# Optimization experiments

Hardware: AMD Instinct MI355X
Metric: run time of the kernel (lower is better)

The kernel has to match this reference:

```python
import jax, jax.numpy as jnp
import numpy as np

ALPHA = 0.2        # LeakyReLU slope
NEG_BIG = -9e15    # mask fill value from the original module


def setup_inputs() -> dict:
    key = jax.random.key(0)
    k1, k2, k3, k4 = jax.random.split(key, 4)
    N, F_IN, F_OUT = 8192, 256, 128
    h = jax.random.normal(k1, (N, F_IN), dtype=jnp.float32)
    adj = jax.random.randint(k2, (N, N), 0, 2, dtype=jnp.int32)
    W = jax.random.normal(k3, (F_IN, F_OUT), dtype=jnp.float32) * (1.0 / np.sqrt(F_IN))
    a = jax.random.normal(k4, (2 * F_OUT, 1), dtype=jnp.float32) * (1.0 / np.sqrt(2 * F_OUT))
    return {"h": h, "adj": adj, "W": W, "a": a}


def reference(h, adj, W, a):
    f_out = W.shape[1]
    Wh = h @ W                                   # [N, F_out]
    Wh1 = Wh @ a[:f_out, :]                      # [N, 1]
    Wh2 = Wh @ a[f_out:, :]                      # [N, 1]
    e = Wh1 + Wh2.T                              # [N, N] broadcast-add
    e = jnp.where(e > 0, e, ALPHA * e)           # LeakyReLU
    e = jnp.where(adj > 0, e, NEG_BIG)           # adjacency mask
    attention = jax.nn.softmax(e, axis=-1)       # row softmax
    # dropout rate = 0.0 -> identity
    h_prime = attention @ Wh                     # [N, F_out]
    return jax.nn.elu(h_prime)
```

## Files before the change

### kernel.cpp

```cpp
#include <hip/hip_runtime.h>

#define NV 8192
#define FIN 256
#define FOUT 128
#define NSPLIT 8
#define SPLITW 1024

typedef __bf16 bf16_t;
typedef __attribute__((ext_vector_type(8))) __bf16 bf16x8;
typedef __attribute__((ext_vector_type(16))) float f32x16;

__global__ __launch_bounds__(256) void wh_kernel(
    const float* __restrict__ h, const float* __restrict__ W,
    const float* __restrict__ a,
    bf16_t* __restrict__ WhbT,
    float* __restrict__ E1, float* __restrict__ F1,
    float* __restrict__ E2, float* __restrict__ F2)
{
  __shared__ float As[64][34];
  __shared__ float Bs[64][128];
  __shared__ float Cs[32][129];
  __shared__ float red1[32][16];
  __shared__ float red2[32][16];
  const int t  = threadIdx.x;
  const int i0 = blockIdx.x * 32;
  const int c  = t & 15;
  const int r  = t >> 4;
  float acc0[8], acc1[8];
  #pragma unroll
  for (int j = 0; j < 8; j++) { acc0[j] = 0.f; acc1[j] = 0.f; }

  for (int k0 = 0; k0 < FIN; k0 += 64) {
    {
      const int ia = t >> 3;
      const int ka = (t & 7) * 8;
      const float* src = h + (size_t)(i0 + ia) * FIN + k0 + ka;
      float4 v0 = *(const float4*)src;
      float4 v1 = *(const float4*)(src + 4);
      As[ka+0][ia]=v0.x; As[ka+1][ia]=v0.y; As[ka+2][ia]=v0.z; As[ka+3][ia]=v0.w;
      As[ka+4][ia]=v1.x; As[ka+5][ia]=v1.y; As[ka+6][ia]=v1.z; As[ka+7][ia]=v1.w;
    }
    {
      const int kb = t >> 2;
      const int cb = (t & 3) * 32;
      const float4* src = (const float4*)(W + (size_t)(k0 + kb) * FOUT + cb);
      float4* dst = (float4*)&Bs[kb][cb];
      #pragma unroll
      for (int q = 0; q < 8; q++) dst[q] = src[q];
    }
    __syncthreads();
    #pragma unroll 4
    for (int k = 0; k < 64; k++) {
      float2 av = *(const float2*)&As[k][r*2];
      float b[8];
      *(float4*)&b[0] = *(const float4*)&Bs[k][c*8];
      *(float4*)&b[4] = *(const float4*)&Bs[k][c*8+4];
      #pragma unroll
      for (int j = 0; j < 8; j++) {
        acc0[j] = fmaf(av.x, b[j], acc0[j]);
        acc1[j] = fmaf(av.y, b[j], acc1[j]);
      }
    }
    __syncthreads();
  }

  float p1a = 0.f, p2a = 0.f, p1b = 0.f, p2b = 0.f;
  #pragma unroll
  for (int j = 0; j < 8; j++) {
    Cs[r*2][c*8+j]   = acc0[j];
    Cs[r*2+1][c*8+j] = acc1[j];
    float w1 = a[c*8+j];
    float w2 = a[FOUT + c*8+j];
    p1a = fmaf(acc0[j], w1, p1a); p2a = fmaf(acc0[j], w2, p2a);
    p1b = fmaf(acc1[j], w1, p1b); p2b = fmaf(acc1[j], w2, p2b);
  }
  red1[r*2][c]   = p1a; red2[r*2][c]   = p2a;
  red1[r*2+1][c] = p1b; red2[r*2+1][c] = p2b;
  __syncthreads();
  if (t < 32) {
    float s = 0.f;
    #pragma unroll
    for (int q = 0; q < 16; q++) s += red1[t][q];
    E1[i0 + t] = __expf(s);
    F1[i0 + t] = __expf(0.2f * s);
  } else if (t < 64) {
    float s = 0.f;
    #pragma unroll
    for (int q = 0; q < 16; q++) s += red2[t-32][q];
    E2[i0 + t - 32] = __expf(s);
    F2[i0 + t - 32] = __expf(0.2f * s);
  }
  {
    const int f = t & 127, half = t >> 7;
    union { bf16_t b[16]; uint4 v[2]; } pk;
    #pragma unroll
    for (int q = 0; q < 16; q++) pk.b[q] = (bf16_t)Cs[half*16 + q][f];
    uint4* dst = (uint4*)(WhbT + (size_t)f * NV + i0 + half*16);
    dst[0] = pk.v[0]; dst[1] = pk.v[1];
  }
}

__global__ __launch_bounds__(256, 3) void attn_kernel(
    const int* __restrict__ adj, const bf16_t* __restrict__ WhbT,
    const float* __restrict__ E1v, const float* __restrict__ F1v,
    const float* __restrict__ E2v, const float* __restrict__ F2v,
    float* __restrict__ nump, float* __restrict__ denp)
{
  __shared__ bf16_t Plds[64][72];
  __shared__ bf16_t Blds[2][128][72];
  __shared__ float denlds[64][4];
  const int t     = threadIdx.x;
  const int rb    = blockIdx.x >> 3;
  const int split = blockIdx.x & 7;
  const int i0 = rb * 64;
  const int j0 = split * SPLITW;
  const int il = t >> 2;
  const int jg = (t & 3) * 16;
  const float e1 = E1v[i0 + il];
  const float f1 = F1v[i0 + il];
  const int lane = t & 63;
  const int w    = t >> 6;
  const int rh = (w & 1) * 32;
  const int ch = (w >> 1) * 64;
  const int ml = lane & 31;
  const int kh = (lane >> 5) * 8;
  f32x16 acc0 = {};
  f32x16 acc1 = {};
  float den_t = 0.f;

  const int bn  = t >> 1;
  const int bhf = (t & 1) * 32;
  const bf16_t* bsrc = WhbT + (size_t)bn * NV + j0 + bhf;
  const int* arow = adj + (size_t)(i0 + il) * NV + j0 + jg;

  uint4 br0, br1, br2, br3;
  {
    const uint4* s4 = (const uint4*)bsrc;
    br0 = s4[0]; br1 = s4[1]; br2 = s4[2]; br3 = s4[3];
  }
  int4 ca0 = *(const int4*)(arow + 0);
  int4 ca1 = *(const int4*)(arow + 4);
  int4 ca2 = *(const int4*)(arow + 8);
  int4 ca3 = *(const int4*)(arow + 12);

  for (int jc = 0; jc < SPLITW; jc += 64) {
    const int jb  = j0 + jc;
    const int buf = (jc >> 6) & 1;
    {
      uint4* bd = (uint4*)&Blds[buf][bn][bhf];
      bd[0] = br0; bd[1] = br1; bd[2] = br2; bd[3] = br3;
    }
    float4 w0 = *(const float4*)(E2v + jb + jg);
    float4 w1 = *(const float4*)(E2v + jb + jg + 4);
    float4 w2 = *(const float4*)(E2v + jb + jg + 8);
    float4 w3 = *(const float4*)(E2v + jb + jg + 12);
    float4 x0 = *(const float4*)(F2v + jb + jg);
    float4 x1 = *(const float4*)(F2v + jb + jg + 4);
    float4 x2 = *(const float4*)(F2v + jb + jg + 8);
    float4 x3 = *(const float4*)(F2v + jb + jg + 12);
    const int jn = (jc + 64 < SPLITW) ? jc + 64 : jc;
    {
      const uint4* s4 = (const uint4*)(bsrc + jn);
      br0 = s4[0]; br1 = s4[1]; br2 = s4[2]; br3 = s4[3];
    }
    const int* nrow = arow + jn;
    int4 na0 = *(const int4*)(nrow + 0);
    int4 na1 = *(const int4*)(nrow + 4);
    int4 na2 = *(const int4*)(nrow + 8);
    int4 na3 = *(const int4*)(nrow + 12);
    {
      bf16x8 pv0, pv1;
      float d0 = 0.f, d1 = 0.f, d2 = 0.f, d3 = 0.f;
      #define PGRP(CA, E4, F4, DD, PV, SL) { \
        float px = fmaxf(e1*E4.x, f1*F4.x); px = (CA.x > 0) ? px : 0.f; DD += px; PV[SL+0] = (bf16_t)px; \
        float py = fmaxf(e1*E4.y, f1*F4.y); py = (CA.y > 0) ? py : 0.f; DD += py; PV[SL+1] = (bf16_t)py; \
        float pz = fmaxf(e1*E4.z, f1*F4.z); pz = (CA.z > 0) ? pz : 0.f; DD += pz; PV[SL+2] = (bf16_t)pz; \
        float pw = fmaxf(e1*E4.w, f1*F4.w); pw = (CA.w > 0) ? pw : 0.f; DD += pw; PV[SL+3] = (bf16_t)pw; }
      PGRP(ca0, w0, x0, d0, pv0, 0)
      PGRP(ca1, w1, x1, d1, pv0, 4)
      PGRP(ca2, w2, x2, d2, pv1, 0)
      PGRP(ca3, w3, x3, d3, pv1, 4)
      #undef PGRP
      den_t += (d0 + d1) + (d2 + d3);
      *(bf16x8*)&Plds[il][jg]     = pv0;
      *(bf16x8*)&Plds[il][jg + 8] = pv1;
    }
    asm volatile("s_waitcnt lgkmcnt(0)\n\ts_barrier" ::: "memory");
    #pragma unroll
    for (int ks = 0; ks < 4; ks++) {
      const int k = ks * 16 + kh;
      bf16x8 af = *(const bf16x8*)&Plds[rh + ml][k];
      bf16x8 b0 = *(const bf16x8*)&Blds[buf][ch + ml][k];
      bf16x8 b1 = *(const bf16x8*)&Blds[buf][ch + 32 + ml][k];
      acc0 = __builtin_amdgcn_mfma_f32_32x32x16_bf16(af, b0, acc0, 0, 0, 0);
      acc1 = __builtin_amdgcn_mfma_f32_32x32x16_bf16(af, b1, acc1, 0, 0, 0);
    }
    asm volatile("s_barrier" ::: "memory");
    ca0 = na0; ca1 = na1; ca2 = na2; ca3 = na3;
  }

  denlds[il][t & 3] = den_t;
  __syncthreads();
  if (t < 64) {
    denp[(size_t)split * NV + i0 + t] =
        denlds[t][0] + denlds[t][1] + denlds[t][2] + denlds[t][3];
  }
  float* base = nump + ((size_t)split * NV + i0) * FOUT;
  const int col = ch + ml;
  const int r4  = 4 * (lane >> 5);
  #pragma unroll
  for (int reg = 0; reg < 16; reg++) {
    const int row = rh + (reg & 3) + 8 * (reg >> 2) + r4;
    base[(size_t)row * FOUT + col]      = acc0[reg];
    base[(size_t)row * FOUT + col + 32] = acc1[reg];
  }
}

__global__ __launch_bounds__(256) void finalize_kernel(
    const float* __restrict__ nump, const float* __restrict__ denp,
    float* __restrict__ out)
{
  const int gid = blockIdx.x * 256 + threadIdx.x;
  const int i  = gid >> 5;
  const int f0 = (gid & 31) * 4;
  float den = 0.f;
  #pragma unroll
  for (int sp = 0; sp < NSPLIT; sp++) den += denp[(size_t)sp * NV + i];
  float4 s = make_float4(0.f, 0.f, 0.f, 0.f);
  #pragma unroll
  for (int sp = 0; sp < NSPLIT; sp++) {
    float4 v = *(const float4*)&nump[((size_t)sp * NV + i) * FOUT + f0];
    s.x += v.x; s.y += v.y; s.z += v.z; s.w += v.w;
  }
  const float inv = 1.0f / den;
  float4 r;
  r.x = s.x * inv; r.y = s.y * inv; r.z = s.z * inv; r.w = s.w * inv;
  r.x = r.x > 0.f ? r.x : __expf(r.x) - 1.0f;
  r.y = r.y > 0.f ? r.y : __expf(r.y) - 1.0f;
  r.z = r.z > 0.f ? r.z : __expf(r.z) - 1.0f;
  r.w = r.w > 0.f ? r.w : __expf(r.w) - 1.0f;
  *(float4*)&out[(size_t)i * FOUT + f0] = r;
}

extern "C" void kernel_launch(void* const* d_in, const int* in_sizes, int n_in,
                              void* d_out, int out_size, void* d_ws, size_t ws_size,
                              hipStream_t stream) {
  const float* h  = (const float*)d_in[0];
  const int*  adj = (const int*)d_in[1];
  const float* W  = (const float*)d_in[2];
  const float* a  = (const float*)d_in[3];
  float* out = (float*)d_out;
  char* ws = (char*)d_ws;
  bf16_t* WhbT = (bf16_t*)ws;
  float* E1   = (float*)(ws + 2097152);
  float* F1   = (float*)(ws + 2129920);
  float* E2   = (float*)(ws + 2162688);
  float* F2   = (float*)(ws + 2195456);
  float* denp = (float*)(ws + 2228224);
  float* nump = (float*)(ws + 2490368);

  wh_kernel<<<256, 256, 0, stream>>>(h, W, a, WhbT, E1, F1, E2, F2);
  attn_kernel<<<1024, 256, 0, stream>>>(adj, WhbT, E1, F1, E2, F2, nump, denp);
  finalize_kernel<<<1024, 256, 0, stream>>>(nump, denp, out);
}
```

Baseline: 417.6 us.

## Pack adjacency mask into bitmask in a separate pass before attention

Adds a pack kernel that converts the int32 adjacency matrix into one bit per edge. The attention kernel then reads one 32-bit word per thread per tile instead of sixteen int32 values, and tests bits for masking. This takes the large adjacency stream out of the MFMA-heavy kernel and lightens its loads and register use. The cost is an extra kernel launch that still reads the full adjacency matrix and writes the bit array to the workspace.

```diff
diff --git a/kernel.cpp b/kernel.cpp
--- a/kernel.cpp
+++ b/kernel.cpp
@@ -5,10 +5,34 @@
 #define FOUT 128
 #define NSPLIT 8
 #define SPLITW 1024
+#define NW32 256
 
 typedef __bf16 bf16_t;
 typedef __attribute__((ext_vector_type(8))) __bf16 bf16x8;
 typedef __attribute__((ext_vector_type(16))) float f32x16;
+
+__global__ __launch_bounds__(256) void pack_kernel(
+    const int* __restrict__ adj, unsigned* __restrict__ bits)
+{
+  const int g0 = (blockIdx.x * 256 + threadIdx.x) * 4;
+  unsigned ob[4];
+  #pragma unroll
+  for (int k = 0; k < 4; k++) {
+    const int* src = adj + (size_t)(g0 + k) * 32;
+    unsigned b = 0;
+    #pragma unroll
+    for (int q = 0; q < 8; q++) {
+      int4 v = *(const int4*)(src + q * 4);
+      b |= (v.x > 0) ? (1u << (q * 4 + 0)) : 0u;
+      b |= (v.y > 0) ? (1u << (q * 4 + 1)) : 0u;
+      b |= (v.z > 0) ? (1u << (q * 4 + 2)) : 0u;
+      b |= (v.w > 0) ? (1u << (q * 4 + 3)) : 0u;
+    }
+    ob[k] = b;
+  }
+  uint4 o = make_uint4(ob[0], ob[1], ob[2], ob[3]);
+  *(uint4*)(bits + g0) = o;
+}
 
 __global__ __launch_bounds__(256) void wh_kernel(
     const float* __restrict__ h, const float* __restrict__ W,
@@ -101,7 +125,7 @@
 }
 
 __global__ __launch_bounds__(256, 3) void attn_kernel(
-    const int* __restrict__ adj, const bf16_t* __restrict__ WhbT,
+    const unsigned* __restrict__ abits, const bf16_t* __restrict__ WhbT,
     const float* __restrict__ E1v, const float* __restrict__ F1v,
     const float* __restrict__ E2v, const float* __restrict__ F2v,
     float* __restrict__ nump, float* __restrict__ denp)
@@ -124,6 +148,7 @@
   const int ch = (w >> 1) * 64;
   const int ml = lane & 31;
   const int kh = (lane >> 5) * 8;
+  const int bb = jg & 16;
   f32x16 acc0 = {};
   f32x16 acc1 = {};
   float den_t = 0.f;
@@ -131,17 +156,14 @@
   const int bn  = t >> 1;
   const int bhf = (t & 1) * 32;
   const bf16_t* bsrc = WhbT + (size_t)bn * NV + j0 + bhf;
-  const int* arow = adj + (size_t)(i0 + il) * NV + j0 + jg;
+  const unsigned* arow32 = abits + (size_t)(i0 + il) * NW32 + ((j0 + jg) >> 5);
 
   uint4 br0, br1, br2, br3;
   {
     const uint4* s4 = (const uint4*)bsrc;
     br0 = s4[0]; br1 = s4[1]; br2 = s4[2]; br3 = s4[3];
   }
-  int4 ca0 = *(const int4*)(arow + 0);
-  int4 ca1 = *(const int4*)(arow + 4);
-  int4 ca2 = *(const int4*)(arow + 8);
-  int4 ca3 = *(const int4*)(arow + 12);
+  unsigned cbits = arow32[0];
 
   for (int jc = 0; jc < SPLITW; jc += 64) {
     const int jb  = j0 + jc;
@@ -163,23 +185,20 @@
       const uint4* s4 = (const uint4*)(bsrc + jn);
       br0 = s4[0]; br1 = s4[1]; br2 = s4[2]; br3 = s4[3];
     }
-    const int* nrow = arow + jn;
-    int4 na0 = *(const int4*)(nrow + 0);
-    int4 na1 = *(const int4*)(nrow + 4);
-    int4 na2 = *(const int4*)(nrow + 8);
-    int4 na3 = *(const int4*)(nrow + 12);
-    {
+    unsigned nbits = arow32[jn >> 5];
+    {
+      const unsigned hb = cbits >> bb;
       bf16x8 pv0, pv1;
       float d0 = 0.f, d1 = 0.f, d2 = 0.f, d3 = 0.f;
-      #define PGRP(CA, E4, F4, DD, PV, SL) { \
-        float px = fmaxf(e1*E4.x, f1*F4.x); px = (CA.x > 0) ? px : 0.f; DD += px; PV[SL+0] = (bf16_t)px; \
-        float py = fmaxf(e1*E4.y, f1*F4.y); py = (CA.y > 0) ? py : 0.f; DD += py; PV[SL+1] = (bf16_t)py; \
-        float pz = fmaxf(e1*E4.z, f1*F4.z); pz = (CA.z > 0) ? pz : 0.f; DD += pz; PV[SL+2] = (bf16_t)pz; \
-        float pw = fmaxf(e1*E4.w, f1*F4.w); pw = (CA.w > 0) ? pw : 0.f; DD += pw; PV[SL+3] = (bf16_t)pw; }
-      PGRP(ca0, w0, x0, d0, pv0, 0)
-      PGRP(ca1, w1, x1, d1, pv0, 4)
-      PGRP(ca2, w2, x2, d2, pv1, 0)
-      PGRP(ca3, w3, x3, d3, pv1, 4)
+      #define PGRP(B, E4, F4, DD, PV, SL) { \
+        float px = fmaxf(e1*E4.x, f1*F4.x); px = (hb & (1u<<(B+0))) ? px : 0.f; DD += px; PV[SL+0] = (bf16_t)px; \
+        float py = fmaxf(e1*E4.y, f1*F4.y); py = (hb & (1u<<(B+1))) ? py : 0.f; DD += py; PV[SL+1] = (bf16_t)py; \
+        float pz = fmaxf(e1*E4.z, f1*F4.z); pz = (hb & (1u<<(B+2))) ? pz : 0.f; DD += pz; PV[SL+2] = (bf16_t)pz; \
+        float pw = fmaxf(e1*E4.w, f1*F4.w); pw = (hb & (1u<<(B+3))) ? pw : 0.f; DD += pw; PV[SL+3] = (bf16_t)pw; }
+      PGRP( 0, w0, x0, d0, pv0, 0)
+      PGRP( 4, w1, x1, d1, pv0, 4)
+      PGRP( 8, w2, x2, d2, pv1, 0)
+      PGRP(12, w3, x3, d3, pv1, 4)
       #undef PGRP
       den_t += (d0 + d1) + (d2 + d3);
       *(bf16x8*)&Plds[il][jg]     = pv0;
@@ -196,7 +215,7 @@
       acc1 = __builtin_amdgcn_mfma_f32_32x32x16_bf16(af, b1, acc1, 0, 0, 0);
     }
     asm volatile("s_barrier" ::: "memory");
-    ca0 = na0; ca1 = na1; ca2 = na2; ca3 = na3;
+    cbits = nbits;
   }
 
   denlds[il][t & 3] = den_t;
@@ -258,8 +277,10 @@
   float* F2   = (float*)(ws + 2195456);
   float* denp = (float*)(ws + 2228224);
   float* nump = (float*)(ws + 2490368);
-
+  unsigned* AdjBits = (unsigned*)(ws + 2490368 + 33554432);
+
+  pack_kernel<<<2048, 256, 0, stream>>>(adj, AdjBits);
   wh_kernel<<<256, 256, 0, stream>>>(h, W, a, WhbT, E1, F1, E2, F2);
-  attn_kernel<<<1024, 256, 0, stream>>>(adj, WhbT, E1, F1, E2, F2, nump, denp);
+  attn_kernel<<<1024, 256, 0, stream>>>(AdjBits, WhbT, E1, F1, E2, F2, nump, denp);
   finalize_kernel<<<1024, 256, 0, stream>>>(nump, denp, out);
 }
```

After: 459.1 us. +9.9%, slower.
